# Performance work log

Hardware: AMD Instinct MI355X
Metric: run time of the kernel (lower is better)

The kernel has to match this reference:

```python
import jax, jax.numpy as jnp
import numpy as np

B, T, I, H, NL, OUT = 64, 512, 128, 512, 2, 24


def _lstm_layer(x_seq, Wih, Whh, bih, bhh):
    # x_seq: [B, T, in_dim]; Wih: [4H, in_dim]; Whh: [4H, H]
    Bsz = x_seq.shape[0]
    Hd = Whh.shape[1]
    # precompute input contribution for all timesteps (one big GEMM)
    xg = jnp.einsum('bti,gi->btg', x_seq, Wih) + bih  # [B, T, 4H]

    def step(carry, xg_t):
        h, c = carry
        g = xg_t + h @ Whh.T + bhh  # [B, 4H]
        i, f, gg, o = jnp.split(g, 4, axis=-1)  # PyTorch gate order: i, f, g, o
        i = jax.nn.sigmoid(i)
        f = jax.nn.sigmoid(f)
        gg = jnp.tanh(gg)
        o = jax.nn.sigmoid(o)
        c = f * c + i * gg
        h = o * jnp.tanh(c)
        return (h, c), h

    h0 = jnp.zeros((Bsz, Hd), x_seq.dtype)
    c0 = jnp.zeros((Bsz, Hd), x_seq.dtype)
    _, hs = jax.lax.scan(step, (h0, c0), jnp.swapaxes(xg, 0, 1))  # hs: [T, B, H]
    return jnp.swapaxes(hs, 0, 1)  # [B, T, H]


def setup_inputs() -> dict:
    key = jax.random.key(0)
    ks = jax.random.split(key, 11)
    s = 1.0 / np.sqrt(H)  # PyTorch LSTM init scale
    return {
        'x': jax.random.normal(ks[0], (B, T, I), jnp.float32),
        'Wih0': jax.random.uniform(ks[1], (4 * H, I), jnp.float32, -s, s),
        'Whh0': jax.random.uniform(ks[2], (4 * H, H), jnp.float32, -s, s),
        'bih0': jax.random.uniform(ks[3], (4 * H,), jnp.float32, -s, s),
        'bhh0': jax.random.uniform(ks[4], (4 * H,), jnp.float32, -s, s),
        'Wih1': jax.random.uniform(ks[5], (4 * H, H), jnp.float32, -s, s),
        'Whh1': jax.random.uniform(ks[6], (4 * H, H), jnp.float32, -s, s),
        'bih1': jax.random.uniform(ks[7], (4 * H,), jnp.float32, -s, s),
        'bhh1': jax.random.uniform(ks[8], (4 * H,), jnp.float32, -s, s),
        'fcW': jax.random.uniform(ks[9], (OUT, H), jnp.float32, -s, s),
        'fcb': jax.random.uniform(ks[10], (OUT,), jnp.float32, -s, s),
    }


def reference(x, Wih0, Whh0, bih0, bhh0, Wih1, Whh1, bih1, bhh1, fcW, fcb):
    h1 = _lstm_layer(x, Wih0, Whh0, bih0, bhh0)   # layer 0: [B, T, H]
    h2 = _lstm_layer(h1, Wih1, Whh1, bih1, bhh1)  # layer 1: [B, T, H]
    last = h2[:, -1, :]                           # [B, H]
    out = last @ fcW.T + fcb                      # [B, 24]
    return out[:, :, None]                        # [B, 24, 1]
```

## Files before the change

### kernel.cpp

```cpp
#include <hip/hip_runtime.h>
#include <math.h>

#define NB 64
#define TT 512
#define IN 128
#define HD 512
#define BGN 4
#define BGB 16
#define RBN 64

__device__ __forceinline__ float sigf(float x) { return 1.0f / (1.0f + expf(-x)); }
__device__ __forceinline__ float dot4(float4 a, float4 b) {
    return a.x*b.x + a.y*b.y + a.z*b.z + a.w*b.w;
}

__device__ __forceinline__ void load_coh16(const float* p,
                                           float4& a, float4& b,
                                           float4& c, float4& d) {
    asm volatile(
        "global_load_dwordx4 %0, %4, off sc0 sc1\n\t"
        "global_load_dwordx4 %1, %4, off offset:16 sc0 sc1\n\t"
        "global_load_dwordx4 %2, %4, off offset:32 sc0 sc1\n\t"
        "global_load_dwordx4 %3, %4, off offset:48 sc0 sc1"
        : "=&v"(a), "=&v"(b), "=&v"(c), "=&v"(d)
        : "v"(p)
        : "memory");
}
__device__ __forceinline__ void wait_vm0() {
    asm volatile("s_waitcnt vmcnt(0)" ::: "memory");
}
__device__ __forceinline__ void store_coh(float* p, float v) {
    asm volatile("global_store_dword %0, %1, off sc0 sc1"
                 :: "v"(p), "v"(v) : "memory");
}
__device__ __forceinline__ int load_coh_int(const int* p) {
    int v;
    asm volatile("global_load_dword %0, %1, off sc0 sc1\n\ts_waitcnt vmcnt(0)"
                 : "=v"(v) : "v"(p) : "memory");
    return v;
}
__device__ __forceinline__ void store_coh_int(int* p, int v) {
    asm volatile("global_store_dword %0, %1, off sc0 sc1"
                 :: "v"(p), "v"(v) : "memory");
}

__device__ __forceinline__ float wave_reduce64(float* A, int l) {
    #pragma unroll
    for (int s = 0; s < 6; ++s) {
        const int m = 1 << s;
        const bool bit = (l >> s) & 1;
        const int cnt = 64 >> (s + 1);
        #pragma unroll
        for (int i = 0; i < cnt; ++i) {
            float send = bit ? A[2*i]     : A[2*i + 1];
            float keep = bit ? A[2*i + 1] : A[2*i];
            float recv = __shfl_xor(send, m, 64);
            A[i] = keep + recv;
        }
    }
    return A[0];
}

__global__ __launch_bounds__(512) void lstm_persist(
    const float* __restrict__ x,
    const float* __restrict__ Wih0, const float* __restrict__ Whh0,
    const float* __restrict__ bih0, const float* __restrict__ bhh0,
    const float* __restrict__ Wih1, const float* __restrict__ Whh1,
    const float* __restrict__ bih1, const float* __restrict__ bhh1,
    const float* __restrict__ fcW, const float* __restrict__ fcb,
    float* __restrict__ ws, float* __restrict__ out)
{
    __shared__ float x_lds[BGB][IN];
    __shared__ float h0_lds[BGB][HD];
    __shared__ float h2_lds[BGB][HD];

    const int tid = threadIdx.x;
    const int l   = tid & 63;
    const int w   = tid >> 6;

    const int xcd  = blockIdx.x & 7;
    const int slot = blockIdx.x >> 3;
    const int rb   = xcd * 8 + (slot >> 2);
    const int bg   = slot & 3;

    const int u   = rb * 8 + w;
    const int us  = __builtin_amdgcn_readfirstlane(u);
    const int bg16 = bg * BGB;
    const int bl   = l & 15;

    float* h0T = ws;
    float* h2T = ws + 2 * HD * NB;
    int*  flags  = (int*)(ws + 4 * HD * NB);
    int*  gslots = flags + bg * 64;

    const float b0i = bih0[0*HD+us] + bhh0[0*HD+us];
    const float b0f = bih0[1*HD+us] + bhh0[1*HD+us];
    const float b0c = bih0[2*HD+us] + bhh0[2*HD+us];
    const float b0o = bih0[3*HD+us] + bhh0[3*HD+us];
    const float b1i = bih1[0*HD+us] + bhh1[0*HD+us];
    const float b1f = bih1[1*HD+us] + bhh1[1*HD+us];
    const float b1c = bih1[2*HD+us] + bhh1[2*HD+us];
    const float b1o = bih1[3*HD+us] + bhh1[3*HD+us];
    const float bias0 = (l & 32) ? ((l & 16) ? b0o : b0c) : ((l & 16) ? b0f : b0i);
    const float bias1 = (l & 32) ? ((l & 16) ? b1o : b1c) : ((l & 16) ? b1f : b1i);

    float c0r = 0.0f, c2r = 0.0f;

    for (int s = 0; s <= TT; ++s) {
        float4 xpf;
        const int xb = tid >> 5, xi = (tid & 31) * 4;
        if (s < TT)
            xpf = *(const float4*)(x + ((size_t)(bg16 + xb) * TT + s) * IN + xi);

        if (s > 0) {
            if (tid < 64) {
                const int* myslot = gslots + l;
                int spins = 0;
                while (!__all(load_coh_int(myslot) >= s)) {
                    __builtin_amdgcn_s_sleep(2);
                    if (++spins > (1 << 18)) break;
                }
            }
            __syncthreads();
        }

        const int cur = s & 1;
        const float* h0prev = h0T + (cur ^ 1) * HD * NB;
        const float* h2prev = h2T + cur * HD * NB;

        {
            const float* s0 = h0prev + (size_t)tid * NB + bg16;
            const float* s2 = h2prev + (size_t)tid * NB + bg16;
            float4 q0, q1, q2, q3, p0, p1, p2, p3;
            load_coh16(s0, q0, q1, q2, q3);
            load_coh16(s2, p0, p1, p2, p3);
            wait_vm0();
            h0_lds[ 0][tid]=q0.x; h0_lds[ 1][tid]=q0.y; h0_lds[ 2][tid]=q0.z; h0_lds[ 3][tid]=q0.w;
            h0_lds[ 4][tid]=q1.x; h0_lds[ 5][tid]=q1.y; h0_lds[ 6][tid]=q1.z; h0_lds[ 7][tid]=q1.w;
            h0_lds[ 8][tid]=q2.x; h0_lds[ 9][tid]=q2.y; h0_lds[10][tid]=q2.z; h0_lds[11][tid]=q2.w;
            h0_lds[12][tid]=q3.x; h0_lds[13][tid]=q3.y; h0_lds[14][tid]=q3.z; h0_lds[15][tid]=q3.w;
            h2_lds[ 0][tid]=p0.x; h2_lds[ 1][tid]=p0.y; h2_lds[ 2][tid]=p0.z; h2_lds[ 3][tid]=p0.w;
            h2_lds[ 4][tid]=p1.x; h2_lds[ 5][tid]=p1.y; h2_lds[ 6][tid]=p1.z; h2_lds[ 7][tid]=p1.w;
            h2_lds[ 8][tid]=p2.x; h2_lds[ 9][tid]=p2.y; h2_lds[10][tid]=p2.z; h2_lds[11][tid]=p2.w;
            h2_lds[12][tid]=p3.x; h2_lds[13][tid]=p3.y; h2_lds[14][tid]=p3.z; h2_lds[15][tid]=p3.w;
            if (s < TT)
                *(float4*)&x_lds[xb][xi] = xpf;
        }
        __syncthreads();

        float r0 = 0.0f, r1 = 0.0f;

        if (s < TT) {
            float A[64];
            #pragma unroll
            for (int j = 0; j < 64; ++j) A[j] = 0.0f;
            #pragma unroll
            for (int b = 0; b < BGB; ++b) {
                float4 ha = *(const float4*)&h0_lds[b][l * 4];
                float4 hb = *(const float4*)&h0_lds[b][256 + l * 4];
                float2 xv = *(const float2*)&x_lds[b][l * 2];
                #pragma unroll
                for (int g = 0; g < 4; ++g) {
                    const size_t r = (size_t)g * HD + us;
                    float4 wa = *(const float4*)(Whh0 + r * HD +       l * 4);
                    float4 wb = *(const float4*)(Whh0 + r * HD + 256 + l * 4);
                    float2 wx = *(const float2*)(Wih0 + r * IN + l * 2);
                    A[g * 16 + b] += dot4(wa, ha) + dot4(wb, hb)
                                   + wx.x * xv.x + wx.y * xv.y;
                }
            }
            r0 = wave_reduce64(A, l) + bias0;
        }
        if (s >= 1) {
            float A[64];
            #pragma unroll
            for (int j = 0; j < 64; ++j) A[j] = 0.0f;
            #pragma unroll
            for (int b = 0; b < BGB; ++b) {
                float4 ha = *(const float4*)&h0_lds[b][l * 4];
                float4 hb = *(const float4*)&h0_lds[b][256 + l * 4];
                float4 qa = *(const float4*)&h2_lds[b][l * 4];
                float4 qb = *(const float4*)&h2_lds[b][256 + l * 4];
                #pragma unroll
                for (int g = 0; g < 4; ++g) {
                    const size_t r = (size_t)g * HD + us;
                    float4 wi0 = *(const float4*)(Wih1 + r * HD +       l * 4);
                    float4 wi1 = *(const float4*)(Wih1 + r * HD + 256 + l * 4);
                    float4 wh0 = *(const float4*)(Whh1 + r * HD +       l * 4);
                    float4 wh1 = *(const float4*)(Whh1 + r * HD + 256 + l * 4);
                    A[g * 16 + b] += dot4(wi0, ha) + dot4(wi1, hb)
                                   + dot4(wh0, qa) + dot4(wh1, qb);
                }
            }
            r1 = wave_reduce64(A, l) + bias1;
        }

        float gi0 = __shfl(r0, bl,      64);
        float gf0 = __shfl(r0, bl + 16, 64);
        float gc0 = __shfl(r0, bl + 32, 64);
        float go0 = __shfl(r0, bl + 48, 64);
        float gi1 = __shfl(r1, bl,      64);
        float gf1 = __shfl(r1, bl + 16, 64);
        float gc1 = __shfl(r1, bl + 32, 64);
        float go1 = __shfl(r1, bl + 48, 64);
        if (l < 16) {
            if (s < TT) {
                float cn = sigf(gf0) * c0r + sigf(gi0) * tanhf(gc0);
                c0r = cn;
                store_coh(h0T + cur * HD * NB + (size_t)us * NB + bg16 + bl,
                          sigf(go0) * tanhf(cn));
            }
            if (s >= 1) {
                float cn = sigf(gf1) * c2r + sigf(gi1) * tanhf(gc1);
                c2r = cn;
                store_coh(h2T + (cur ^ 1) * HD * NB + (size_t)us * NB + bg16 + bl,
                          sigf(go1) * tanhf(cn));
            }
        }

        __syncthreads();
        if (tid == 0) store_coh_int(gslots + rb, s + 1);
    }

    if (rb != 0) return;
    {
        if (tid < 64) {
            const int* myslot = gslots + l;
            int spins = 0;
            while (!__all(load_coh_int(myslot) >= TT + 1)) {
                __builtin_amdgcn_s_sleep(2);
                if (++spins > (1 << 18)) break;
            }
        }
        __syncthreads();

        const float* hsrc = h2T + 1 * HD * NB + (size_t)tid * NB + bg16;
        float4 q0, q1, q2, q3;
        load_coh16(hsrc, q0, q1, q2, q3);
        wait_vm0();
        h2_lds[ 0][tid]=q0.x; h2_lds[ 1][tid]=q0.y; h2_lds[ 2][tid]=q0.z; h2_lds[ 3][tid]=q0.w;
        h2_lds[ 4][tid]=q1.x; h2_lds[ 5][tid]=q1.y; h2_lds[ 6][tid]=q1.z; h2_lds[ 7][tid]=q1.w;
        h2_lds[ 8][tid]=q2.x; h2_lds[ 9][tid]=q2.y; h2_lds[10][tid]=q2.z; h2_lds[11][tid]=q2.w;
        h2_lds[12][tid]=q3.x; h2_lds[13][tid]=q3.y; h2_lds[14][tid]=q3.z; h2_lds[15][tid]=q3.w;
        __syncthreads();

        const int bb = tid >> 5, oo = tid & 31;
        if (oo < 24) {
            float acc = fcb[oo];
            const float4* hrow = (const float4*)&h2_lds[bb][0];
            const float4* wrow = (const float4*)(fcW + (size_t)oo * HD);
            #pragma unroll 8
            for (int q = 0; q < HD / 4; ++q) acc += dot4(hrow[q], wrow[q]);
            out[(size_t)(bg16 + bb) * 24 + oo] = acc;
        }
    }
}

extern "C" void kernel_launch(void* const* d_in, const int* in_sizes, int n_in,
                              void* d_out, int out_size, void* d_ws, size_t ws_size,
                              hipStream_t stream)
{
    const float* x    = (const float*)d_in[0];
    const float* Wih0 = (const float*)d_in[1];
    const float* Whh0 = (const float*)d_in[2];
    const float* bih0 = (const float*)d_in[3];
    const float* bhh0 = (const float*)d_in[4];
    const float* Wih1 = (const float*)d_in[5];
    const float* Whh1 = (const float*)d_in[6];
    const float* bih1 = (const float*)d_in[7];
    const float* bhh1 = (const float*)d_in[8];
    const float* fcW  = (const float*)d_in[9];
    const float* fcb  = (const float*)d_in[10];

    hipMemsetAsync(d_ws, 0, (size_t)(4 * HD * NB) * sizeof(float) + 1024, stream);

    lstm_persist<<<dim3(BGN * RBN), dim3(512), 0, stream>>>(
        x, Wih0, Whh0, bih0, bhh0, Wih1, Whh1, bih1, bhh1, fcW, fcb,
        (float*)d_ws, (float*)d_out);
}
```

Baseline: 7.366 ms.

## Overlap input projection with coherent h loads and prefetch x after signaling

Moves the x-timestep load to after the step's completion flag is published, so it no longer sits on the critical path before the spin-wait. The Wih0·x partial products are computed while the coherent h-state loads are in flight, hiding their latency before the wait. All waves now spin on the flags instead of only the first wave, and the old barrier that followed the spin now runs every step. This trades extra polling traffic and one more barrier per step for less latency on the serial recurrence chain.

```diff
diff --git a/kernel.cpp b/kernel.cpp
--- a/kernel.cpp
+++ b/kernel.cpp
@@ -106,27 +106,28 @@
 
     float c0r = 0.0f, c2r = 0.0f;
 
+    const int xb = tid >> 5, xi = (tid & 31) * 4;
+    {
+        float4 xp = *(const float4*)(x + ((size_t)(bg16 + xb) * TT + 0) * IN + xi);
+        *(float4*)&x_lds[xb][xi] = xp;
+    }
+
     for (int s = 0; s <= TT; ++s) {
-        float4 xpf;
-        const int xb = tid >> 5, xi = (tid & 31) * 4;
-        if (s < TT)
-            xpf = *(const float4*)(x + ((size_t)(bg16 + xb) * TT + s) * IN + xi);
-
         if (s > 0) {
-            if (tid < 64) {
-                const int* myslot = gslots + l;
-                int spins = 0;
-                while (!__all(load_coh_int(myslot) >= s)) {
-                    __builtin_amdgcn_s_sleep(2);
-                    if (++spins > (1 << 18)) break;
-                }
-            }
-            __syncthreads();
-        }
+            const int* myslot = gslots + l;
+            int spins = 0;
+            while (!__all(load_coh_int(myslot) >= s)) {
+                __builtin_amdgcn_s_sleep(2);
+                if (++spins > (1 << 18)) break;
+            }
+        }
+        __syncthreads();
 
         const int cur = s & 1;
         const float* h0prev = h0T + (cur ^ 1) * HD * NB;
         const float* h2prev = h2T + cur * HD * NB;
+
+        float A[64];
 
         {
             const float* s0 = h0prev + (size_t)tid * NB + bg16;
@@ -134,6 +135,22 @@
             float4 q0, q1, q2, q3, p0, p1, p2, p3;
             load_coh16(s0, q0, q1, q2, q3);
             load_coh16(s2, p0, p1, p2, p3);
+
+            if (s < TT) {
+                float2 wx0 = *(const float2*)(Wih0 + ((size_t)0*HD+us) * IN + l*2);
+                float2 wx1 = *(const float2*)(Wih0 + ((size_t)1*HD+us) * IN + l*2);
+                float2 wx2 = *(const float2*)(Wih0 + ((size_t)2*HD+us) * IN + l*2);
+                float2 wx3 = *(const float2*)(Wih0 + ((size_t)3*HD+us) * IN + l*2);
+                #pragma unroll
+                for (int b = 0; b < BGB; ++b) {
+                    float2 xv = *(const float2*)&x_lds[b][l * 2];
+                    A[ 0 + b] = wx0.x * xv.x + wx0.y * xv.y;
+                    A[16 + b] = wx1.x * xv.x + wx1.y * xv.y;
+                    A[32 + b] = wx2.x * xv.x + wx2.y * xv.y;
+                    A[48 + b] = wx3.x * xv.x + wx3.y * xv.y;
+                }
+            }
+
             wait_vm0();
             h0_lds[ 0][tid]=q0.x; h0_lds[ 1][tid]=q0.y; h0_lds[ 2][tid]=q0.z; h0_lds[ 3][tid]=q0.w;
             h0_lds[ 4][tid]=q1.x; h0_lds[ 5][tid]=q1.y; h0_lds[ 6][tid]=q1.z; h0_lds[ 7][tid]=q1.w;
@@ -143,36 +160,27 @@
             h2_lds[ 4][tid]=p1.x; h2_lds[ 5][tid]=p1.y; h2_lds[ 6][tid]=p1.z; h2_lds[ 7][tid]=p1.w;
             h2_lds[ 8][tid]=p2.x; h2_lds[ 9][tid]=p2.y; h2_lds[10][tid]=p2.z; h2_lds[11][tid]=p2.w;
             h2_lds[12][tid]=p3.x; h2_lds[13][tid]=p3.y; h2_lds[14][tid]=p3.z; h2_lds[15][tid]=p3.w;
-            if (s < TT)
-                *(float4*)&x_lds[xb][xi] = xpf;
         }
         __syncthreads();
 
         float r0 = 0.0f, r1 = 0.0f;
 
         if (s < TT) {
-            float A[64];
-            #pragma unroll
-            for (int j = 0; j < 64; ++j) A[j] = 0.0f;
             #pragma unroll
             for (int b = 0; b < BGB; ++b) {
                 float4 ha = *(const float4*)&h0_lds[b][l * 4];
                 float4 hb = *(const float4*)&h0_lds[b][256 + l * 4];
-                float2 xv = *(const float2*)&x_lds[b][l * 2];
                 #pragma unroll
                 for (int g = 0; g < 4; ++g) {
                     const size_t r = (size_t)g * HD + us;
                     float4 wa = *(const float4*)(Whh0 + r * HD +       l * 4);
                     float4 wb = *(const float4*)(Whh0 + r * HD + 256 + l * 4);
-                    float2 wx = *(const float2*)(Wih0 + r * IN + l * 2);
-                    A[g * 16 + b] += dot4(wa, ha) + dot4(wb, hb)
-                                   + wx.x * xv.x + wx.y * xv.y;
+                    A[g * 16 + b] += dot4(wa, ha) + dot4(wb, hb);
                 }
             }
             r0 = wave_reduce64(A, l) + bias0;
         }
         if (s >= 1) {
-            float A[64];
             #pragma unroll
             for (int j = 0; j < 64; ++j) A[j] = 0.0f;
             #pragma unroll
@@ -220,6 +228,11 @@
 
         __syncthreads();
         if (tid == 0) store_coh_int(gslots + rb, s + 1);
+
+        if (s + 1 < TT) {
+            float4 xp = *(const float4*)(x + ((size_t)(bg16 + xb) * TT + (s + 1)) * IN + xi);
+            *(float4*)&x_lds[xb][xi] = xp;
+        }
     }
 
     if (rb != 0) return;
```

Measured after the change: 13.91 ms. +88.9%, slower.
